# Kernel tuning notes

Hardware: AMD Instinct MI355X
Metric: run time of the kernel (lower is better)

## Reference

```python
import jax, jax.numpy as jnp
import numpy as np

B, N, E, IN = 16, 4096, 65536, 128
FILTERS = [256, 256, 128]


def setup_inputs() -> dict:
    key = jax.random.key(0)
    ks = jax.random.split(key, 12)
    inp = {
        "x": jax.random.normal(ks[0], (B, N, IN), dtype=jnp.float32),
        "edge_index": jax.random.randint(ks[1], (B, 2, E), 0, N, dtype=jnp.int32),
        "edge_weight": jax.random.uniform(ks[2], (B, E), dtype=jnp.float32),
        "mask": jax.random.randint(ks[3], (B, N), 0, 2, dtype=jnp.int32),
    }
    dims = [IN] + FILTERS
    for i in range(3):
        inp[f"W{i+1}"] = jax.random.normal(ks[4 + 2 * i], (dims[i], dims[i + 1]), dtype=jnp.float32) / np.sqrt(dims[i]).astype(np.float32)
        inp[f"b{i+1}"] = 0.01 * jax.random.normal(ks[5 + 2 * i], (dims[i + 1],), dtype=jnp.float32)
    return inp


def _gcn_layer(x, ei, ew, valid, W, b):
    # GCNConv(add_self_loops=False, normalize=False):
    #   h = x @ W; out[v] = sum_{(u,v)} ew * h[u]; out += b (valid rows only)
    h = x @ W  # [N, d_out]
    u, v = ei[0], ei[1]
    evalid = valid[u] & valid[v]            # drop edges touching masked-out nodes
    w = jnp.where(evalid, ew, 0.0)
    agg = jnp.zeros_like(h).at[v].add(w[:, None] * h[u])
    return jnp.where(valid[:, None], agg + b, 0.0)


def reference(x, edge_index, edge_weight, mask, W1, b1, W2, b2, W3, b3):
    valid = mask > 0  # [B, N] bool
    out = x
    for W, b in ((W1, b1), (W2, b2), (W3, b3)):
        out = jax.vmap(_gcn_layer, in_axes=(0, 0, 0, 0, None, None))(
            out, edge_index, edge_weight, valid, W, b)
        out = jax.nn.relu(out)  # dropout p=0.0 -> identity
    return out
```

## Files before the change

kernel.cpp:

```cpp
#include <hip/hip_runtime.h>

static constexpr int BATCH = 16;
static constexpr int NNODE = 4096;
static constexpr int NEDGE = 65536;
static constexpr int ROWS  = BATCH * NNODE;
static constexpr int CAP   = 2432;
static constexpr int PM    = BATCH * CAP;
static constexpr int DCAP  = 64;

typedef _Float16 half8  __attribute__((ext_vector_type(8)));
typedef _Float16 half4v __attribute__((ext_vector_type(4)));
typedef _Float16 half2v __attribute__((ext_vector_type(2)));
typedef float    f32x4  __attribute__((ext_vector_type(4)));
typedef float    f32x2  __attribute__((ext_vector_type(2)));

__global__ __launch_bounds__(256) void build_kernel(
    const int* __restrict__ ei, const float* __restrict__ ew,
    const int* __restrict__ mask, const float* __restrict__ X,
    const float* __restrict__ W1, const float* __restrict__ W2,
    const float* __restrict__ W3,
    int* __restrict__ cursor, unsigned int* __restrict__ bkt,
    _Float16* __restrict__ X16, _Float16* __restrict__ Wt1,
    _Float16* __restrict__ Wt2, _Float16* __restrict__ Wt3,
    int* __restrict__ vlist, int* __restrict__ validN)
{
    __shared__ int sums[256];
    const int blk = blockIdx.x;
    const int t   = threadIdx.x;

    if (blk < 4096) {
        const int idx = blk * 256 + t;
        const int b = idx >> 16;
        const int e = idx & (NEDGE - 1);
        const int* eib = ei + (size_t)b * 2 * NEDGE;
        const int u = eib[e];
        const int v = eib[NEDGE + e];
        const int mrow = b * NNODE;
        if (mask[mrow + u] != 0 && mask[mrow + v] != 0) {
            const _Float16 w = (_Float16)ew[(size_t)b * NEDGE + e];
            const unsigned short wb = __builtin_bit_cast(unsigned short, w);
            const int pos = atomicAdd(&cursor[mrow + v], 1);
            if (pos < DCAP)
                bkt[(size_t)(mrow + v) * DCAP + pos] = ((unsigned)wb << 16) | (unsigned)u;
        }
    } else if (blk < 12288) {
        const int i = (blk - 4096) * 256 + t;
        const int row = i >> 5;
        const int c4  = i & 31;
        const float4 s = *(const float4*)&X[(size_t)row * 128 + c4 * 4];
        half4v h = {(_Float16)s.x, (_Float16)s.y, (_Float16)s.z, (_Float16)s.w};
        *(half4v*)&X16[(size_t)row * 128 + c4 * 4] = h;
    } else if (blk < 12800) {
        const int i = (blk - 12288) * 256 + t;
        if (i < 32768) {
            int k = i >> 8, n = i & 255;
            Wt1[n * 128 + k] = (_Float16)W1[i];
        } else if (i < 98304) {
            int j = i - 32768;
            int k = j >> 8, n = j & 255;
            Wt2[n * 256 + k] = (_Float16)W2[j];
        } else {
            int j = i - 98304;
            int k = j >> 7, n = j & 127;
            Wt3[n * 256 + k] = (_Float16)W3[j];
        }
    } else {
        const int b = blk - 12800;
        const int* mb = mask + b * NNODE;
        for (int i = t; i < CAP; i += 256) vlist[b * CAP + i] = 0;

        int loc[16]; int s = 0;
        #pragma unroll
        for (int i = 0; i < 16; ++i) { loc[i] = (mb[t * 16 + i] != 0); s += loc[i]; }
        sums[t] = s;
        __syncthreads();
        for (int off = 1; off < 256; off <<= 1) {
            int v = (t >= off) ? sums[t - off] : 0;
            __syncthreads();
            sums[t] += v;
            __syncthreads();
        }
        int run = (t == 0) ? 0 : sums[t - 1];
        #pragma unroll
        for (int i = 0; i < 16; ++i) {
            const int n = t * 16 + i;
            if (loc[i]) {
                if (run < CAP) vlist[b * CAP + run] = n;
                ++run;
            }
        }
        if (t == 255) validN[b] = run;
    }
}

__global__ __launch_bounds__(256, 3) void fused_g1(
    const unsigned int* __restrict__ bkt, const int* __restrict__ cursor,
    const _Float16* __restrict__ X16,
    const int* __restrict__ vlist, const int* __restrict__ validN,
    const _Float16* __restrict__ Wt,
    const float* __restrict__ bias,
    _Float16* __restrict__ Ac)
{
    constexpr int K = 128, N = 256;
    constexpr int NPAN = K / 32;
    constexpr int NW   = N / 4;
    constexpr int NI   = NW / 16;
    constexpr int RST  = NW + 8;
    constexpr int NCH  = CAP / 64;
    __shared__ _Float16 A16[NPAN * 2048];

    const int tid  = threadIdx.x;
    const int lane = tid & 63;
    const int wave = tid >> 6;
    const int quad = lane >> 4;
    const int l15  = lane & 15;

    const int xcd  = blockIdx.x & 7;
    const int j    = blockIdx.x >> 3;
    const int batch = 2 * xcd + (j >= NCH);
    const int tile  = (j >= NCH) ? j - NCH : j;
    const int vN   = validN[batch];
    if (tile * 64 >= vN) return;
    const int mrow = batch * NNODE;
    const _Float16* Xb = X16 + (size_t)mrow * 128 + lane * 2;

    for (int r = 0; r < 16; ++r) {
        const int slot = tile * 64 + wave * 16 + r;
        float a0 = 0.0f, a1 = 0.0f;
        if (slot < vN) {
            const int v = vlist[batch * CAP + slot];
            int deg = cursor[mrow + v];
            deg = deg > DCAP ? DCAP : deg;
            const unsigned* bk = bkt + (size_t)(mrow + v) * DCAP;
            for (int i = 0; i < deg; i += 8) {
                const int cnt = deg - i;
                unsigned pk[8];
                #pragma unroll
                for (int tt = 0; tt < 8; ++tt) pk[tt] = bk[i + tt];
                const unsigned u0 = pk[0] & 0xffffu;
                float wj[8]; const _Float16* hp[8];
                #pragma unroll
                for (int tt = 0; tt < 8; ++tt) {
                    const bool ok = (tt < cnt);
                    const unsigned u = ok ? (pk[tt] & 0xffffu) : u0;
                    wj[tt] = ok ? (float)__builtin_bit_cast(_Float16, (unsigned short)(pk[tt] >> 16)) : 0.0f;
                    hp[tt] = Xb + (size_t)u * 128;
                }
                half2v hv[8];
                #pragma unroll
                for (int tt = 0; tt < 8; ++tt) hv[tt] = *(const half2v*)hp[tt];
                #pragma unroll
                for (int tt = 0; tt < 8; ++tt) {
                    a0 += wj[tt] * (float)hv[tt][0];
                    a1 += wj[tt] * (float)hv[tt][1];
                }
            }
        }
        const int row = wave * 16 + r;
        half2v o = {(_Float16)a0, (_Float16)a1};
        *(half2v*)&A16[quad * 2048 + row * 32 + l15 * 2] = o;
    }
    __syncthreads();

    f32x4 acc[4][NI];
    #pragma unroll
    for (int mi = 0; mi < 4; ++mi)
        #pragma unroll
        for (int ni = 0; ni < NI; ++ni) acc[mi][ni] = (f32x4)0.0f;

    const _Float16* ap = A16 + l15 * 32 + quad * 8;
    const _Float16* wp = Wt + (size_t)(wave * NW + l15) * K + quad * 8;

    #pragma unroll
    for (int pp = 0; pp < NPAN; ++pp) {
        half8 af[4], bf[NI];
        #pragma unroll
        for (int mi = 0; mi < 4; ++mi)
            af[mi] = *(const half8*)(ap + pp * 2048 + mi * 16 * 32);
        #pragma unroll
        for (int ni = 0; ni < NI; ++ni)
            bf[ni] = *(const half8*)(wp + (size_t)ni * 16 * K + pp * 32);
        #pragma unroll
        for (int mi = 0; mi < 4; ++mi)
            #pragma unroll
            for (int ni = 0; ni < NI; ++ni)
                acc[mi][ni] = __builtin_amdgcn_mfma_f32_16x16x32_f16(
                    bf[ni], af[mi], acc[mi][ni], 0, 0, 0);
    }
    __syncthreads();

    _Float16* stg = A16 + wave * 16 * RST;
    const int rr = lane >> 2;
    const int c0 = lane & 3;
    #pragma unroll
    for (int mi = 0; mi < 4; ++mi) {
        #pragma unroll
        for (int ni = 0; ni < NI; ++ni) {
            f32x4 v = acc[mi][ni];
            const f32x4 bv = *(const f32x4*)&bias[wave * NW + ni * 16 + quad * 4];
            half4v o;
            #pragma unroll
            for (int r = 0; r < 4; ++r) o[r] = (_Float16)fmaxf(v[r] + bv[r], 0.0f);
            *(half4v*)&stg[l15 * RST + ni * 16 + quad * 4] = o;
        }
        const int slot = tile * 64 + mi * 16 + rr;
        if (slot < vN) {
            const int vs = vlist[batch * CAP + slot];
            _Float16* hp2 = &Ac[((size_t)mrow + vs) * 256 + wave * NW];
            #pragma unroll
            for (int c = 0; c < NI / 2; ++c) {
                const int ch = (c0 + 4 * c) * 8;
                half8 v = *(const half8*)&stg[rr * RST + ch];
                *(half8*)(hp2 + ch) = v;
            }
        }
    }
}

__global__ __launch_bounds__(256, 3) void fused_g23(
    const unsigned int* __restrict__ bkt, const int* __restrict__ cursor,
    const _Float16* __restrict__ Ac,
    const int* __restrict__ vlist, const int* __restrict__ validN,
    const _Float16* __restrict__ Wt2,
    const _Float16* __restrict__ Wt3,
    const float* __restrict__ b2,
    _Float16* __restrict__ H3)
{
    constexpr int K    = 256;
    constexpr int NPAN = 8;
    constexpr int NCH  = CAP / 64;
    __shared__ _Float16 A16[NPAN * 2048];

    const int tid  = threadIdx.x;
    const int lane = tid & 63;
    const int wave = tid >> 6;
    const int quad = lane >> 4;
    const int l15  = lane & 15;

    const int xcd  = blockIdx.x & 7;
    const int j    = blockIdx.x >> 3;
    const int batch = 2 * xcd + (j >= NCH);
    const int tile  = (j >= NCH) ? j - NCH : j;
    const int vN   = validN[batch];
    if (tile * 64 >= vN) return;
    const int mrow = batch * NNODE;
    const _Float16* Ab = Ac + (size_t)mrow * 256 + lane * 4;

    for (int r = 0; r < 16; ++r) {
        const int slot = tile * 64 + wave * 16 + r;
        float a0 = 0.0f, a1 = 0.0f, a2 = 0.0f, a3 = 0.0f;
        if (slot < vN) {
            const int v = vlist[batch * CAP + slot];
            int deg = cursor[mrow + v];
            deg = deg > DCAP ? DCAP : deg;
            const unsigned* bk = bkt + (size_t)(mrow + v) * DCAP;
            for (int i = 0; i < deg; i += 8) {
                const int cnt = deg - i;
                unsigned pk[8];
                #pragma unroll
                for (int tt = 0; tt < 8; ++tt) pk[tt] = bk[i + tt];
                const unsigned u0 = pk[0] & 0xffffu;
                float wj[8]; const _Float16* hp[8];
                #pragma unroll
                for (int tt = 0; tt < 8; ++tt) {
                    const bool ok = (tt < cnt);
                    const unsigned u = ok ? (pk[tt] & 0xffffu) : u0;
                    wj[tt] = ok ? (float)__builtin_bit_cast(_Float16, (unsigned short)(pk[tt] >> 16)) : 0.0f;
                    hp[tt] = Ab + (size_t)u * 256;
                }
                half4v hv[8];
                #pragma unroll
                for (int tt = 0; tt < 8; ++tt) hv[tt] = *(const half4v*)hp[tt];
                #pragma unroll
                for (int tt = 0; tt < 8; ++tt) {
                    a0 += wj[tt] * (float)hv[tt][0];
                    a1 += wj[tt] * (float)hv[tt][1];
                    a2 += wj[tt] * (float)hv[tt][2];
                    a3 += wj[tt] * (float)hv[tt][3];
                }
            }
        }
        const int row = wave * 16 + r;
        half4v o = {(_Float16)a0, (_Float16)a1, (_Float16)a2, (_Float16)a3};
        *(half4v*)&A16[(lane >> 3) * 2048 + row * 32 + ((lane * 4) & 31)] = o;
    }
    __syncthreads();

    f32x4 acc[4][4];
    #pragma unroll
    for (int mi = 0; mi < 4; ++mi)
        #pragma unroll
        for (int ni = 0; ni < 4; ++ni) acc[mi][ni] = (f32x4)0.0f;

    const _Float16* ap = A16 + l15 * 32 + quad * 8;
    const _Float16* wp = Wt2 + (size_t)(wave * 64 + l15) * K + quad * 8;

    #pragma unroll
    for (int pp = 0; pp < NPAN; ++pp) {
        half8 af[4], bf[4];
        #pragma unroll
        for (int mi = 0; mi < 4; ++mi)
            af[mi] = *(const half8*)(ap + pp * 2048 + mi * 16 * 32);
        #pragma unroll
        for (int ni = 0; ni < 4; ++ni)
            bf[ni] = *(const half8*)(wp + (size_t)ni * 16 * K + pp * 32);
        #pragma unroll
        for (int mi = 0; mi < 4; ++mi)
            #pragma unroll
            for (int ni = 0; ni < 4; ++ni)
                acc[mi][ni] = __builtin_amdgcn_mfma_f32_16x16x32_f16(
                    bf[ni], af[mi], acc[mi][ni], 0, 0, 0);
    }
    __syncthreads();

    #pragma unroll
    for (int mi = 0; mi < 4; ++mi) {
        const int row = mi * 16 + l15;
        #pragma unroll
        for (int ni = 0; ni < 4; ++ni) {
            const int col = wave * 64 + ni * 16 + quad * 4;
            const f32x4 bv = *(const f32x4*)&b2[col];
            f32x4 v = acc[mi][ni];
            half4v o;
            #pragma unroll
            for (int r = 0; r < 4; ++r) o[r] = (_Float16)fmaxf(v[r] + bv[r], 0.0f);
            *(half4v*)&A16[(col >> 5) * 2048 + row * 32 + (col & 31)] = o;
        }
    }
    __syncthreads();

    f32x4 acc2[4][2];
    #pragma unroll
    for (int mi = 0; mi < 4; ++mi)
        #pragma unroll
        for (int ni = 0; ni < 2; ++ni) acc2[mi][ni] = (f32x4)0.0f;

    const _Float16* wp3 = Wt3 + (size_t)(wave * 32 + l15) * K + quad * 8;
    #pragma unroll
    for (int pp = 0; pp < NPAN; ++pp) {
        half8 af[4], bf[2];
        #pragma unroll
        for (int mi = 0; mi < 4; ++mi)
            af[mi] = *(const half8*)(ap + pp * 2048 + mi * 16 * 32);
        #pragma unroll
        for (int ni = 0; ni < 2; ++ni)
            bf[ni] = *(const half8*)(wp3 + (size_t)ni * 16 * K + pp * 32);
        #pragma unroll
        for (int mi = 0; mi < 4; ++mi)
            #pragma unroll
            for (int ni = 0; ni < 2; ++ni)
                acc2[mi][ni] = __builtin_amdgcn_mfma_f32_16x16x32_f16(
                    bf[ni], af[mi], acc2[mi][ni], 0, 0, 0);
    }
    __syncthreads();

    constexpr int RST = 40;
    _Float16* stg = A16 + wave * 16 * RST;
    const int rr = lane >> 2;
    const int c0 = lane & 3;
    #pragma unroll
    for (int mi = 0; mi < 4; ++mi) {
        #pragma unroll
        for (int ni = 0; ni < 2; ++ni) {
            f32x4 v = acc2[mi][ni];
            half4v o;
            #pragma unroll
            for (int r = 0; r < 4; ++r) o[r] = (_Float16)v[r];
            *(half4v*)&stg[l15 * RST + ni * 16 + quad * 4] = o;
        }
        const int slot = tile * 64 + mi * 16 + rr;
        if (slot < vN) {
            const int vs = vlist[batch * CAP + slot];
            _Float16* hp2 = &H3[((size_t)mrow + vs) * 128 + wave * 32];
            const int ch = c0 * 8;
            half8 v = *(const half8*)&stg[rr * RST + ch];
            *(half8*)(hp2 + ch) = v;
        }
    }
}

__global__ __launch_bounds__(256) void gather_final(
    const int* __restrict__ cursor, const unsigned int* __restrict__ bkt,
    const _Float16* __restrict__ H3,
    const int* __restrict__ mask, const float* __restrict__ bias,
    float* __restrict__ OUT)
{
    constexpr int NU = NNODE / 4;
    const int tid  = threadIdx.x;
    const int lane = tid & 63;
    const int wave = tid >> 6;

    const int xcd  = blockIdx.x & 7;
    const int jj   = blockIdx.x >> 3;
    const int batch = 2 * xcd + (jj >= NU);
    const int unit  = (jj >= NU) ? jj - NU : jj;

    const int n = unit * 4 + wave;
    const int mrow = batch * NNODE + n;

    float acc[2] = {};
    if (mask[mrow] != 0) {
        int deg = cursor[mrow];
        deg = deg > DCAP ? DCAP : deg;
        const unsigned* bk = bkt + (size_t)mrow * DCAP;
        const _Float16* Hb = H3 + (size_t)batch * NNODE * 128 + lane * 2;

        for (int i = 0; i < deg; i += 8) {
            const int cnt = deg - i;
            unsigned pk[8];
            #pragma unroll
            for (int t = 0; t < 8; ++t) pk[t] = bk[i + t];
            const unsigned u0 = pk[0] & 0xffffu;
            float wj[8]; const _Float16* hp[8];
            #pragma unroll
            for (int t = 0; t < 8; ++t) {
                const bool ok = (t < cnt);
                const unsigned u = ok ? (pk[t] & 0xffffu) : u0;
                wj[t] = ok ? (float)__builtin_bit_cast(_Float16, (unsigned short)(pk[t] >> 16)) : 0.0f;
                hp[t] = Hb + (size_t)u * 128;
            }
            half2v hv[8];
            #pragma unroll
            for (int t = 0; t < 8; ++t) hv[t] = *(const half2v*)hp[t];
            #pragma unroll
            for (int t = 0; t < 8; ++t)
                #pragma unroll
                for (int c = 0; c < 2; ++c) acc[c] += wj[t] * (float)hv[t][c];
        }
        #pragma unroll
        for (int c = 0; c < 2; ++c)
            acc[c] = fmaxf(acc[c] + bias[lane * 2 + c], 0.0f);
    }
    f32x2 o = {acc[0], acc[1]};
    *(f32x2*)&OUT[(size_t)mrow * 128 + lane * 2] = o;
}

extern "C" void kernel_launch(void* const* d_in, const int* in_sizes, int n_in,
                              void* d_out, int out_size, void* d_ws, size_t ws_size,
                              hipStream_t stream) {
    const float* x    = (const float*)d_in[0];
    const int*   ei   = (const int*)  d_in[1];
    const float* ew   = (const float*)d_in[2];
    const int*   mask = (const int*)  d_in[3];
    const float* W1   = (const float*)d_in[4];
    const float* b1   = (const float*)d_in[5];
    const float* W2   = (const float*)d_in[6];
    const float* b2   = (const float*)d_in[7];
    const float* W3   = (const float*)d_in[8];
    const float* b3   = (const float*)d_in[9];
    float* out = (float*)d_out;

    char* ws = (char*)d_ws;
    _Float16* X16 = (_Float16*)(ws);
    _Float16* Ac  = (_Float16*)(ws + (16u << 20));
    _Float16* H3  = (_Float16*)(ws + (48u << 20));
    unsigned int* bkt = (unsigned int*)(ws + (64u << 20));
    _Float16* Wt1 = (_Float16*)(ws + (80u << 20));
    _Float16* Wt2 = Wt1 + 128 * 256;
    _Float16* Wt3 = Wt2 + 256 * 256;
    int* cursor   = (int*)(Wt3 + 256 * 128);
    int* vlist    = cursor + ROWS;
    int* validN   = vlist + PM;

    const dim3 blk(256);

    hipMemsetAsync(cursor, 0, (size_t)ROWS * sizeof(int), stream);

    build_kernel<<<12816, blk, 0, stream>>>(ei, ew, mask, x, W1, W2, W3,
                                            cursor, bkt, X16, Wt1, Wt2, Wt3,
                                            vlist, validN);

    const int gemmBlocks = PM / 64;
    const int finBlocks  = ROWS / 4;

    fused_g1<<<gemmBlocks, blk, 0, stream>>>(bkt, cursor, X16, vlist, validN,
                                             Wt1, b1, Ac);

    fused_g23<<<gemmBlocks, blk, 0, stream>>>(bkt, cursor, Ac, vlist, validN,
                                              Wt2, Wt3, b2, H3);

    gather_final<<<finBlocks, blk, 0, stream>>>(cursor, bkt, H3, mask, b3, out);
}
```

Baseline: 221.5 us.

## Gather fp32 X directly, halve GEMM tile rows, stage bucket heads in LDS

Drops the separate X-to-fp16 conversion pass from the build kernel, so layer 1 gathers fp32 features straight from the input and skips writing and re-reading a 16 MB fp16 copy. Both fused aggregate+GEMM kernels now process 32 rows per block instead of 64, doubling the block count, raising the occupancy hint to 4, and padding LDS panels to reduce bank conflicts. The first 16 bucket entries per row are prefetched into shared memory and gathered in a single unrolled batch, with a scalar tail for higher degrees. The cost is twice as many weight-fragment loads per output row, and wider fp32 gathers in layer 1.

```diff
diff --git a/kernel.cpp b/kernel.cpp
--- a/kernel.cpp
+++ b/kernel.cpp
@@ -16,12 +16,12 @@
 
 __global__ __launch_bounds__(256) void build_kernel(
     const int* __restrict__ ei, const float* __restrict__ ew,
-    const int* __restrict__ mask, const float* __restrict__ X,
+    const int* __restrict__ mask,
     const float* __restrict__ W1, const float* __restrict__ W2,
     const float* __restrict__ W3,
     int* __restrict__ cursor, unsigned int* __restrict__ bkt,
-    _Float16* __restrict__ X16, _Float16* __restrict__ Wt1,
-    _Float16* __restrict__ Wt2, _Float16* __restrict__ Wt3,
+    _Float16* __restrict__ Wt1, _Float16* __restrict__ Wt2,
+    _Float16* __restrict__ Wt3,
     int* __restrict__ vlist, int* __restrict__ validN)
 {
     __shared__ int sums[256];
@@ -43,15 +43,8 @@
             if (pos < DCAP)
                 bkt[(size_t)(mrow + v) * DCAP + pos] = ((unsigned)wb << 16) | (unsigned)u;
         }
-    } else if (blk < 12288) {
+    } else if (blk < 4608) {
         const int i = (blk - 4096) * 256 + t;
-        const int row = i >> 5;
-        const int c4  = i & 31;
-        const float4 s = *(const float4*)&X[(size_t)row * 128 + c4 * 4];
-        half4v h = {(_Float16)s.x, (_Float16)s.y, (_Float16)s.z, (_Float16)s.w};
-        *(half4v*)&X16[(size_t)row * 128 + c4 * 4] = h;
-    } else if (blk < 12800) {
-        const int i = (blk - 12288) * 256 + t;
         if (i < 32768) {
             int k = i >> 8, n = i & 255;
             Wt1[n * 128 + k] = (_Float16)W1[i];
@@ -65,7 +58,7 @@
             Wt3[n * 256 + k] = (_Float16)W3[j];
         }
     } else {
-        const int b = blk - 12800;
+        const int b = blk - 4608;
         const int* mb = mask + b * NNODE;
         for (int i = t; i < CAP; i += 256) vlist[b * CAP + i] = 0;
 
@@ -93,21 +86,23 @@
     }
 }
 
-__global__ __launch_bounds__(256, 3) void fused_g1(
+__global__ __launch_bounds__(256, 4) void fused_g1(
     const unsigned int* __restrict__ bkt, const int* __restrict__ cursor,
-    const _Float16* __restrict__ X16,
+    const float* __restrict__ X,
     const int* __restrict__ vlist, const int* __restrict__ validN,
     const _Float16* __restrict__ Wt,
     const float* __restrict__ bias,
     _Float16* __restrict__ Ac)
 {
-    constexpr int K = 128, N = 256;
-    constexpr int NPAN = K / 32;
-    constexpr int NW   = N / 4;
-    constexpr int NI   = NW / 16;
-    constexpr int RST  = NW + 8;
-    constexpr int NCH  = CAP / 64;
-    __shared__ _Float16 A16[NPAN * 2048];
+    constexpr int K = 128;
+    constexpr int NPAN = 4;
+    constexpr int PSTR = 1032;
+    constexpr int NW = 64, NI = 4, RST = 72;
+    constexpr int NCH = CAP / 32;
+    constexpr int ASZ = (NPAN * PSTR) > (4 * 16 * RST) ? (NPAN * PSTR) : (4 * 16 * RST);
+    __shared__ _Float16 A16[ASZ];
+    __shared__ int s_v[32], s_deg[32];
+    __shared__ unsigned s_bk[32][16];
 
     const int tid  = threadIdx.x;
     const int lane = tid & 63;
@@ -120,51 +115,65 @@
     const int batch = 2 * xcd + (j >= NCH);
     const int tile  = (j >= NCH) ? j - NCH : j;
     const int vN   = validN[batch];
-    if (tile * 64 >= vN) return;
+    if (tile * 32 >= vN) return;
     const int mrow = batch * NNODE;
-    const _Float16* Xb = X16 + (size_t)mrow * 128 + lane * 2;
-
-    for (int r = 0; r < 16; ++r) {
-        const int slot = tile * 64 + wave * 16 + r;
+
+    if (tid < 32) {
+        const int slot = tile * 32 + tid;
+        int v = 0, dg = 0;
+        if (slot < vN) {
+            v = vlist[batch * CAP + slot];
+            dg = cursor[mrow + v];
+            dg = dg > DCAP ? DCAP : dg;
+        }
+        s_v[tid] = v; s_deg[tid] = dg;
+    }
+    __syncthreads();
+    if (tid < 128) {
+        const int r = tid >> 2, part = tid & 3;
+        const uint4 q = *(const uint4*)&bkt[(size_t)(mrow + s_v[r]) * DCAP + part * 4];
+        *(uint4*)&s_bk[r][part * 4] = q;
+    }
+    __syncthreads();
+
+    const float* Xb = X + (size_t)mrow * 128 + lane * 2;
+    for (int r8 = 0; r8 < 8; ++r8) {
+        const int r = wave * 8 + r8;
+        const int dg = s_deg[r];
         float a0 = 0.0f, a1 = 0.0f;
-        if (slot < vN) {
-            const int v = vlist[batch * CAP + slot];
-            int deg = cursor[mrow + v];
-            deg = deg > DCAP ? DCAP : deg;
-            const unsigned* bk = bkt + (size_t)(mrow + v) * DCAP;
-            for (int i = 0; i < deg; i += 8) {
-                const int cnt = deg - i;
-                unsigned pk[8];
-                #pragma unroll
-                for (int tt = 0; tt < 8; ++tt) pk[tt] = bk[i + tt];
-                const unsigned u0 = pk[0] & 0xffffu;
-                float wj[8]; const _Float16* hp[8];
-                #pragma unroll
-                for (int tt = 0; tt < 8; ++tt) {
-                    const bool ok = (tt < cnt);
-                    const unsigned u = ok ? (pk[tt] & 0xffffu) : u0;
-                    wj[tt] = ok ? (float)__builtin_bit_cast(_Float16, (unsigned short)(pk[tt] >> 16)) : 0.0f;
-                    hp[tt] = Xb + (size_t)u * 128;
+        if (dg > 0) {
+            unsigned pk[16];
+            #pragma unroll
+            for (int t = 0; t < 16; ++t) pk[t] = s_bk[r][t];
+            const unsigned u0 = pk[0] & 0xffffu;
+            float wj[16]; float2 xv[16];
+            #pragma unroll
+            for (int t = 0; t < 16; ++t) {
+                const bool ok = (t < dg);
+                const unsigned u = ok ? (pk[t] & 0xffffu) : u0;
+                wj[t] = ok ? (float)__builtin_bit_cast(_Float16, (unsigned short)(pk[t] >> 16)) : 0.0f;
+                xv[t] = *(const float2*)(Xb + (size_t)u * 128);
+            }
+            #pragma unroll
+            for (int t = 0; t < 16; ++t) { a0 += wj[t] * xv[t].x; a1 += wj[t] * xv[t].y; }
+            if (dg > 16) {
+                const unsigned* bk = bkt + (size_t)(mrow + s_v[r]) * DCAP;
+                for (int i = 16; i < dg; ++i) {
+                    const unsigned p = bk[i];
+                    const float w = (float)__builtin_bit_cast(_Float16, (unsigned short)(p >> 16));
+                    const float2 x2 = *(const float2*)(Xb + (size_t)(p & 0xffffu) * 128);
+                    a0 += w * x2.x; a1 += w * x2.y;
                 }
-                half2v hv[8];
-                #pragma unroll
-                for (int tt = 0; tt < 8; ++tt) hv[tt] = *(const half2v*)hp[tt];
-                #pragma unroll
-                for (int tt = 0; tt < 8; ++tt) {
-                    a0 += wj[tt] * (float)hv[tt][0];
-                    a1 += wj[tt] * (float)hv[tt][1];
-                }
-            }
-        }
-        const int row = wave * 16 + r;
+            }
+        }
         half2v o = {(_Float16)a0, (_Float16)a1};
-        *(half2v*)&A16[quad * 2048 + row * 32 + l15 * 2] = o;
-    }
-    __syncthreads();
-
-    f32x4 acc[4][NI];
-    #pragma unroll
-    for (int mi = 0; mi < 4; ++mi)
+        *(half2v*)&A16[(lane >> 4) * PSTR + r * 32 + ((lane * 2) & 31)] = o;
+    }
+    __syncthreads();
+
+    f32x4 acc[2][NI];
+    #pragma unroll
+    for (int mi = 0; mi < 2; ++mi)
         #pragma unroll
         for (int ni = 0; ni < NI; ++ni) acc[mi][ni] = (f32x4)0.0f;
 
@@ -173,15 +182,15 @@
 
     #pragma unroll
     for (int pp = 0; pp < NPAN; ++pp) {
-        half8 af[4], bf[NI];
-        #pragma unroll
-        for (int mi = 0; mi < 4; ++mi)
-            af[mi] = *(const half8*)(ap + pp * 2048 + mi * 16 * 32);
+        half8 af[2], bf[NI];
+        #pragma unroll
+        for (int mi = 0; mi < 2; ++mi)
+            af[mi] = *(const half8*)(ap + pp * PSTR + mi * 16 * 32);
         #pragma unroll
         for (int ni = 0; ni < NI; ++ni)
             bf[ni] = *(const half8*)(wp + (size_t)ni * 16 * K + pp * 32);
         #pragma unroll
-        for (int mi = 0; mi < 4; ++mi)
+        for (int mi = 0; mi < 2; ++mi)
             #pragma unroll
             for (int ni = 0; ni < NI; ++ni)
                 acc[mi][ni] = __builtin_amdgcn_mfma_f32_16x16x32_f16(
@@ -193,7 +202,7 @@
     const int rr = lane >> 2;
     const int c0 = lane & 3;
     #pragma unroll
-    for (int mi = 0; mi < 4; ++mi) {
+    for (int mi = 0; mi < 2; ++mi) {
         #pragma unroll
         for (int ni = 0; ni < NI; ++ni) {
             f32x4 v = acc[mi][ni];
@@ -203,9 +212,9 @@
             for (int r = 0; r < 4; ++r) o[r] = (_Float16)fmaxf(v[r] + bv[r], 0.0f);
             *(half4v*)&stg[l15 * RST + ni * 16 + quad * 4] = o;
         }
-        const int slot = tile * 64 + mi * 16 + rr;
+        const int slot = tile * 32 + mi * 16 + rr;
         if (slot < vN) {
-            const int vs = vlist[batch * CAP + slot];
+            const int vs = s_v[mi * 16 + rr];
             _Float16* hp2 = &Ac[((size_t)mrow + vs) * 256 + wave * NW];
             #pragma unroll
             for (int c = 0; c < NI / 2; ++c) {
@@ -217,7 +226,7 @@
     }
 }
 
-__global__ __launch_bounds__(256, 3) void fused_g23(
+__global__ __launch_bounds__(256, 4) void fused_g23(
     const unsigned int* __restrict__ bkt, const int* __restrict__ cursor,
     const _Float16* __restrict__ Ac,
     const int* __restrict__ vlist, const int* __restrict__ validN,
@@ -228,8 +237,11 @@
 {
     constexpr int K    = 256;
     constexpr int NPAN = 8;
-    constexpr int NCH  = CAP / 64;
-    __shared__ _Float16 A16[NPAN * 2048];
+    constexpr int PSTR = 1032;
+    constexpr int NCH  = CAP / 32;
+    __shared__ _Float16 A16[NPAN * PSTR];
+    __shared__ int s_v[32], s_deg[32];
+    __shared__ unsigned s_bk[32][16];
 
     const int tid  = threadIdx.x;
     const int lane = tid & 63;
@@ -242,53 +254,71 @@
     const int batch = 2 * xcd + (j >= NCH);
     const int tile  = (j >= NCH) ? j - NCH : j;
     const int vN   = validN[batch];
-    if (tile * 64 >= vN) return;
+    if (tile * 32 >= vN) return;
     const int mrow = batch * NNODE;
+
+    if (tid < 32) {
+        const int slot = tile * 32 + tid;
+        int v = 0, dg = 0;
+        if (slot < vN) {
+            v = vlist[batch * CAP + slot];
+            dg = cursor[mrow + v];
+            dg = dg > DCAP ? DCAP : dg;
+        }
+        s_v[tid] = v; s_deg[tid] = dg;
+    }
+    __syncthreads();
+    if (tid < 128) {
+        const int r = tid >> 2, part = tid & 3;
+        const uint4 q = *(const uint4*)&bkt[(size_t)(mrow + s_v[r]) * DCAP + part * 4];
+        *(uint4*)&s_bk[r][part * 4] = q;
+    }
+    __syncthreads();
+
     const _Float16* Ab = Ac + (size_t)mrow * 256 + lane * 4;
-
-    for (int r = 0; r < 16; ++r) {
-        const int slot = tile * 64 + wave * 16 + r;
+    for (int r8 = 0; r8 < 8; ++r8) {
+        const int r = wave * 8 + r8;
+        const int dg = s_deg[r];
         float a0 = 0.0f, a1 = 0.0f, a2 = 0.0f, a3 = 0.0f;
-        if (slot < vN) {
-            const int v = vlist[batch * CAP + slot];
-            int deg = cursor[mrow + v];
-            deg = deg > DCAP ? DCAP : deg;
-            const unsigned* bk = bkt + (size_t)(mrow + v) * DCAP;
-            for (int i = 0; i < deg; i += 8) {
-                const int cnt = deg - i;
-                unsigned pk[8];
-                #pragma unroll
-                for (int tt = 0; tt < 8; ++tt) pk[tt] = bk[i + tt];
-                const unsigned u0 = pk[0] & 0xffffu;
-                float wj[8]; const _Float16* hp[8];
-                #pragma unroll
-                for (int tt = 0; tt < 8; ++tt) {
-                    const bool ok = (tt < cnt);
-                    const unsigned u = ok ? (pk[tt] & 0xffffu) : u0;
-                    wj[tt] = ok ? (float)__builtin_bit_cast(_Float16, (unsigned short)(pk[tt] >> 16)) : 0.0f;
-                    hp[tt] = Ab + (size_t)u * 256;
+        if (dg > 0) {
+            unsigned pk[16];
+            #pragma unroll
+            for (int t = 0; t < 16; ++t) pk[t] = s_bk[r][t];
+            const unsigned u0 = pk[0] & 0xffffu;
+            float wj[16]; half4v hv[16];
+            #pragma unroll
+            for (int t = 0; t < 16; ++t) {
+                const bool ok = (t < dg);
+                const unsigned u = ok ? (pk[t] & 0xffffu) : u0;
+                wj[t] = ok ? (float)__builtin_bit_cast(_Float16, (unsigned short)(pk[t] >> 16)) : 0.0f;
+                hv[t] = *(const half4v*)(Ab + (size_t)u * 256);
+            }
+            #pragma unroll
+            for (int t = 0; t < 16; ++t) {
+                a0 += wj[t] * (float)hv[t][0];
+                a1 += wj[t] * (float)hv[t][1];
+                a2 += wj[t] * (float)hv[t][2];
+                a3 += wj[t] * (float)hv[t][3];
+            }
+            if (dg > 16) {
+                const unsigned* bk = bkt + (size_t)(mrow + s_v[r]) * DCAP;
+                for (int i = 16; i < dg; ++i) {
+                    const unsigned p = bk[i];
+                    const float w = (float)__builtin_bit_cast(_Float16, (unsigned short)(p >> 16));
+                    const half4v h = *(const half4v*)(Ab + (size_t)(p & 0xffffu) * 256);
+                    a0 += w * (float)h[0]; a1 += w * (float)h[1];
+                    a2 += w * (float)h[2]; a3 += w * (float)h[3];
                 }
-                half4v hv[8];
-                #pragma unroll
-                for (int tt = 0; tt < 8; ++tt) hv[tt] = *(const half4v*)hp[tt];
-                #pragma unroll
-                for (int tt = 0; tt < 8; ++tt) {
-                    a0 += wj[tt] * (float)hv[tt][0];
-                    a1 += wj[tt] * (float)hv[tt][1];
-                    a2 += wj[tt] * (float)hv[tt][2];
-                    a3 += wj[tt] * (float)hv[tt][3];
-                }
-            }
-        }
-        const int row = wave * 16 + r;
+            }
+        }
         half4v o = {(_Float16)a0, (_Float16)a1, (_Float16)a2, (_Float16)a3};
-        *(half4v*)&A16[(lane >> 3) * 2048 + row * 32 + ((lane * 4) & 31)] = o;
-    }
-    __syncthreads();
-
-    f32x4 acc[4][4];
-    #pragma unroll
-    for (int mi = 0; mi < 4; ++mi)
+        *(half4v*)&A16[(lane >> 3) * PSTR + r * 32 + ((lane * 4) & 31)] = o;
+    }
+    __syncthreads();
+
+    f32x4 acc[2][4];
+    #pragma unroll
+    for (int mi = 0; mi < 2; ++mi)
         #pragma unroll
         for (int ni = 0; ni < 4; ++ni) acc[mi][ni] = (f32x4)0.0f;
 
@@ -297,15 +327,15 @@
 
     #pragma unroll
     for (int pp = 0; pp < NPAN; ++pp) {
-        half8 af[4], bf[4];
-        #pragma unroll
-        for (int mi = 0; mi < 4; ++mi)
-            af[mi] = *(const half8*)(ap + pp * 2048 + mi * 16 * 32);
+        half8 af[2], bf[4];
+        #pragma unroll
+        for (int mi = 0; mi < 2; ++mi)
+            af[mi] = *(const half8*)(ap + pp * PSTR + mi * 16 * 32);
         #pragma unroll
         for (int ni = 0; ni < 4; ++ni)
             bf[ni] = *(const half8*)(wp + (size_t)ni * 16 * K + pp * 32);
         #pragma unroll
-        for (int mi = 0; mi < 4; ++mi)
+        for (int mi = 0; mi < 2; ++mi)
             #pragma unroll
             for (int ni = 0; ni < 4; ++ni)
                 acc[mi][ni] = __builtin_amdgcn_mfma_f32_16x16x32_f16(
@@ -314,7 +344,7 @@
     __syncthreads();
 
     #pragma unroll
-    for (int mi = 0; mi < 4; ++mi) {
+    for (int mi = 0; mi < 2; ++mi) {
         const int row = mi * 16 + l15;
         #pragma unroll
         for (int ni = 0; ni < 4; ++ni) {
@@ -324,29 +354,29 @@
             half4v o;
             #pragma unroll
             for (int r = 0; r < 4; ++r) o[r] = (_Float16)fmaxf(v[r] + bv[r], 0.0f);
-            *(half4v*)&A16[(col >> 5) * 2048 + row * 32 + (col & 31)] = o;
-        }
-    }
-    __syncthreads();
-
-    f32x4 acc2[4][2];
-    #pragma unroll
-    for (int mi = 0; mi < 4; ++mi)
+            *(half4v*)&A16[(col >> 5) * PSTR + row * 32 + (col & 31)] = o;
+        }
+    }
+    __syncthreads();
+
+    f32x4 acc2[2][2];
+    #pragma unroll
+    for (int mi = 0; mi < 2; ++mi)
         #pragma unroll
         for (int ni = 0; ni < 2; ++ni) acc2[mi][ni] = (f32x4)0.0f;
 
     const _Float16* wp3 = Wt3 + (size_t)(wave * 32 + l15) * K + quad * 8;
     #pragma unroll
     for (int pp = 0; pp < NPAN; ++pp) {
-        half8 af[4], bf[2];
-        #pragma unroll
-        for (int mi = 0; mi < 4; ++mi)
-            af[mi] = *(const half8*)(ap + pp * 2048 + mi * 16 * 32);
+        half8 af[2], bf[2];
+        #pragma unroll
+        for (int mi = 0; mi < 2; ++mi)
+            af[mi] = *(const half8*)(ap + pp * PSTR + mi * 16 * 32);
         #pragma unroll
         for (int ni = 0; ni < 2; ++ni)
             bf[ni] = *(const half8*)(wp3 + (size_t)ni * 16 * K + pp * 32);
         #pragma unroll
-        for (int mi = 0; mi < 4; ++mi)
+        for (int mi = 0; mi < 2; ++mi)
             #pragma unroll
             for (int ni = 0; ni < 2; ++ni)
                 acc2[mi][ni] = __builtin_amdgcn_mfma_f32_16x16x32_f16(
@@ -359,7 +389,7 @@
     const int rr = lane >> 2;
     const int c0 = lane & 3;
     #pragma unroll
-    for (int mi = 0; mi < 4; ++mi) {
+    for (int mi = 0; mi < 2; ++mi) {
         #pragma unroll
         for (int ni = 0; ni < 2; ++ni) {
             f32x4 v = acc2[mi][ni];
@@ -368,9 +398,9 @@
             for (int r = 0; r < 4; ++r) o[r] = (_Float16)v[r];
             *(half4v*)&stg[l15 * RST + ni * 16 + quad * 4] = o;
         }
-        const int slot = tile * 64 + mi * 16 + rr;
+        const int slot = tile * 32 + mi * 16 + rr;
         if (slot < vN) {
-            const int vs = vlist[batch * CAP + slot];
+            const int vs = s_v[mi * 16 + rr];
             _Float16* hp2 = &H3[((size_t)mrow + vs) * 128 + wave * 32];
             const int ch = c0 * 8;
             half8 v = *(const half8*)&stg[rr * RST + ch];
@@ -451,11 +481,10 @@
     float* out = (float*)d_out;
 
     char* ws = (char*)d_ws;
-    _Float16* X16 = (_Float16*)(ws);
-    _Float16* Ac  = (_Float16*)(ws + (16u << 20));
-    _Float16* H3  = (_Float16*)(ws + (48u << 20));
-    unsigned int* bkt = (unsigned int*)(ws + (64u << 20));
-    _Float16* Wt1 = (_Float16*)(ws + (80u << 20));
+    _Float16* Ac  = (_Float16*)(ws);
+    _Float16* H3  = (_Float16*)(ws + (32u << 20));
+    unsigned int* bkt = (unsigned int*)(ws + (48u << 20));
+    _Float16* Wt1 = (_Float16*)(ws + (64u << 20));
     _Float16* Wt2 = Wt1 + 128 * 256;
     _Float16* Wt3 = Wt2 + 256 * 256;
     int* cursor   = (int*)(Wt3 + 256 * 128);
@@ -466,14 +495,14 @@
 
     hipMemsetAsync(cursor, 0, (size_t)ROWS * sizeof(int), stream);
 
-    build_kernel<<<12816, blk, 0, stream>>>(ei, ew, mask, x, W1, W2, W3,
-                                            cursor, bkt, X16, Wt1, Wt2, Wt3,
-                                            vlist, validN);
-
-    const int gemmBlocks = PM / 64;
+    build_kernel<<<4624, blk, 0, stream>>>(ei, ew, mask, W1, W2, W3,
+                                           cursor, bkt, Wt1, Wt2, Wt3,
+                                           vlist, validN);
+
+    const int gemmBlocks = PM / 32;
     const int finBlocks  = ROWS / 4;
 
-    fused_g1<<<gemmBlocks, blk, 0, stream>>>(bkt, cursor, X16, vlist, validN,
+    fused_g1<<<gemmBlocks, blk, 0, stream>>>(bkt, cursor, x, vlist, validN,
                                              Wt1, b1, Ac);
 
     fused_g23<<<gemmBlocks, blk, 0, stream>>>(bkt, cursor, Ac, vlist, validN,
```

After: 220.7 us. Within noise of the previous version (-0.3%).

## Split neighbor gather out of fused GEMM kernels into separate gather passes

Applied to the files above, without the earlier changes.

Each fused gather+GEMM kernel is split in two. A standalone gather kernel (one wave per valid node) writes the aggregated rows to a compact buffer. The GEMM kernel then loads that buffer into LDS with global_load_lds, and vlist lookups are cached in shared memory. The fp32-to-fp16 conversion of X is removed: the first gather reads fp32 X directly, and the build kernel shrinks to match. Padding lanes now load index-masked rows instead of duplicating the first neighbor. This spreads the latency-bound gather across many more waves, in exchange for two extra launches and an HBM round trip for the aggregated intermediates.

```diff
diff --git a/kernel.cpp b/kernel.cpp
--- a/kernel.cpp
+++ b/kernel.cpp
@@ -14,14 +14,17 @@
 typedef float    f32x4  __attribute__((ext_vector_type(4)));
 typedef float    f32x2  __attribute__((ext_vector_type(2)));
 
+#define GP(p) (const __attribute__((address_space(1))) void*)(p)
+#define LP(p) (__attribute__((address_space(3))) void*)(p)
+
 __global__ __launch_bounds__(256) void build_kernel(
     const int* __restrict__ ei, const float* __restrict__ ew,
-    const int* __restrict__ mask, const float* __restrict__ X,
+    const int* __restrict__ mask,
     const float* __restrict__ W1, const float* __restrict__ W2,
     const float* __restrict__ W3,
     int* __restrict__ cursor, unsigned int* __restrict__ bkt,
-    _Float16* __restrict__ X16, _Float16* __restrict__ Wt1,
-    _Float16* __restrict__ Wt2, _Float16* __restrict__ Wt3,
+    _Float16* __restrict__ Wt1, _Float16* __restrict__ Wt2,
+    _Float16* __restrict__ Wt3,
     int* __restrict__ vlist, int* __restrict__ validN)
 {
     __shared__ int sums[256];
@@ -43,15 +46,8 @@
             if (pos < DCAP)
                 bkt[(size_t)(mrow + v) * DCAP + pos] = ((unsigned)wb << 16) | (unsigned)u;
         }
-    } else if (blk < 12288) {
+    } else if (blk < 4608) {
         const int i = (blk - 4096) * 256 + t;
-        const int row = i >> 5;
-        const int c4  = i & 31;
-        const float4 s = *(const float4*)&X[(size_t)row * 128 + c4 * 4];
-        half4v h = {(_Float16)s.x, (_Float16)s.y, (_Float16)s.z, (_Float16)s.w};
-        *(half4v*)&X16[(size_t)row * 128 + c4 * 4] = h;
-    } else if (blk < 12800) {
-        const int i = (blk - 12288) * 256 + t;
         if (i < 32768) {
             int k = i >> 8, n = i & 255;
             Wt1[n * 128 + k] = (_Float16)W1[i];
@@ -65,7 +61,7 @@
             Wt3[n * 256 + k] = (_Float16)W3[j];
         }
     } else {
-        const int b = blk - 12800;
+        const int b = blk - 4608;
         const int* mb = mask + b * NNODE;
         for (int i = t; i < CAP; i += 256) vlist[b * CAP + i] = 0;
 
@@ -93,21 +89,113 @@
     }
 }
 
-__global__ __launch_bounds__(256, 3) void fused_g1(
-    const unsigned int* __restrict__ bkt, const int* __restrict__ cursor,
-    const _Float16* __restrict__ X16,
+
+__global__ __launch_bounds__(256) void gather_x(
+    const int* __restrict__ cursor, const unsigned int* __restrict__ bkt,
+    const float* __restrict__ X,
+    const int* __restrict__ vlist, const int* __restrict__ validN,
+    _Float16* __restrict__ AggX)
+{
+    constexpr int NU = CAP / 4;
+    const int lane = threadIdx.x & 63;
+    const int wave = threadIdx.x >> 6;
+    const int xcd  = blockIdx.x & 7;
+    const int jj   = blockIdx.x >> 3;
+    const int batch = 2 * xcd + (jj >= NU);
+    const int unit  = (jj >= NU) ? jj - NU : jj;
+
+    const int j = unit * 4 + wave;
+    if (j >= validN[batch]) return;
+    const int mrow = batch * NNODE;
+    const int v = vlist[batch * CAP + j];
+    int deg = cursor[mrow + v];
+    deg = deg > DCAP ? DCAP : deg;
+    const unsigned* bk = bkt + (size_t)(mrow + v) * DCAP;
+    const float* Xb = X + (size_t)mrow * 128 + lane * 2;
+
+    float a0 = 0.0f, a1 = 0.0f;
+    for (int i = 0; i < deg; i += 8) {
+        const int cnt = deg - i;
+        unsigned pk[8];
+        #pragma unroll
+        for (int t = 0; t < 8; ++t) pk[t] = bk[i + t];
+        float wj[8]; float2 xv[8];
+        #pragma unroll
+        for (int t = 0; t < 8; ++t) {
+            const bool ok = (t < cnt);
+            const unsigned u = pk[t] & 0xFFFu;
+            wj[t] = ok ? (float)__builtin_bit_cast(_Float16, (unsigned short)(pk[t] >> 16)) : 0.0f;
+            xv[t] = *(const float2*)(Xb + (size_t)u * 128);
+        }
+        #pragma unroll
+        for (int t = 0; t < 8; ++t) { a0 += wj[t] * xv[t].x; a1 += wj[t] * xv[t].y; }
+    }
+    half2v o = {(_Float16)a0, (_Float16)a1};
+    *(half2v*)&AggX[(size_t)(batch * CAP + j) * 128 + lane * 2] = o;
+}
+
+__global__ __launch_bounds__(256) void gather_agg(
+    const int* __restrict__ cursor, const unsigned int* __restrict__ bkt,
+    const _Float16* __restrict__ Ac,
+    const int* __restrict__ vlist, const int* __restrict__ validN,
+    _Float16* __restrict__ AggA)
+{
+    constexpr int NU = CAP / 4;
+    const int lane = threadIdx.x & 63;
+    const int wave = threadIdx.x >> 6;
+    const int xcd  = blockIdx.x & 7;
+    const int jj   = blockIdx.x >> 3;
+    const int batch = 2 * xcd + (jj >= NU);
+    const int unit  = (jj >= NU) ? jj - NU : jj;
+
+    const int j = unit * 4 + wave;
+    if (j >= validN[batch]) return;
+    const int mrow = batch * NNODE;
+    const int v = vlist[batch * CAP + j];
+    int deg = cursor[mrow + v];
+    deg = deg > DCAP ? DCAP : deg;
+    const unsigned* bk = bkt + (size_t)(mrow + v) * DCAP;
+    const _Float16* Ab = Ac + (size_t)mrow * 256 + lane * 4;
+
+    float a0 = 0.0f, a1 = 0.0f, a2 = 0.0f, a3 = 0.0f;
+    for (int i = 0; i < deg; i += 8) {
+        const int cnt = deg - i;
+        unsigned pk[8];
+        #pragma unroll
+        for (int t = 0; t < 8; ++t) pk[t] = bk[i + t];
+        float wj[8]; half4v hv[8];
+        #pragma unroll
+        for (int t = 0; t < 8; ++t) {
+            const bool ok = (t < cnt);
+            const unsigned u = pk[t] & 0xFFFu;
+            wj[t] = ok ? (float)__builtin_bit_cast(_Float16, (unsigned short)(pk[t] >> 16)) : 0.0f;
+            hv[t] = *(const half4v*)(Ab + (size_t)u * 256);
+        }
+        #pragma unroll
+        for (int t = 0; t < 8; ++t) {
+            a0 += wj[t] * (float)hv[t][0];
+            a1 += wj[t] * (float)hv[t][1];
+            a2 += wj[t] * (float)hv[t][2];
+            a3 += wj[t] * (float)hv[t][3];
+        }
+    }
+    half4v o = {(_Float16)a0, (_Float16)a1, (_Float16)a2, (_Float16)a3};
+    *(half4v*)&AggA[(size_t)(batch * CAP + j) * 256 + lane * 4] = o;
+}
+
+__global__ __launch_bounds__(256, 3) void gemm1_kernel(
+    const _Float16* __restrict__ Xc,
     const int* __restrict__ vlist, const int* __restrict__ validN,
     const _Float16* __restrict__ Wt,
     const float* __restrict__ bias,
     _Float16* __restrict__ Ac)
 {
-    constexpr int K = 128, N = 256;
-    constexpr int NPAN = K / 32;
-    constexpr int NW   = N / 4;
-    constexpr int NI   = NW / 16;
-    constexpr int RST  = NW + 8;
+    constexpr int K = 128, NW = 64, NI = 4, RST = 72;
+    constexpr int NPAN = 4;
     constexpr int NCH  = CAP / 64;
-    __shared__ _Float16 A16[NPAN * 2048];
+    constexpr int ASZ  = (NPAN * 2048) > (4 * 16 * RST) ? (NPAN * 2048) : (4 * 16 * RST);
+    __shared__ _Float16 A16[ASZ];
+    __shared__ int s_v[64];
 
     const int tid  = threadIdx.x;
     const int lane = tid & 63;
@@ -122,44 +210,19 @@
     const int vN   = validN[batch];
     if (tile * 64 >= vN) return;
     const int mrow = batch * NNODE;
-    const _Float16* Xb = X16 + (size_t)mrow * 128 + lane * 2;
-
-    for (int r = 0; r < 16; ++r) {
-        const int slot = tile * 64 + wave * 16 + r;
-        float a0 = 0.0f, a1 = 0.0f;
-        if (slot < vN) {
-            const int v = vlist[batch * CAP + slot];
-            int deg = cursor[mrow + v];
-            deg = deg > DCAP ? DCAP : deg;
-            const unsigned* bk = bkt + (size_t)(mrow + v) * DCAP;
-            for (int i = 0; i < deg; i += 8) {
-                const int cnt = deg - i;
-                unsigned pk[8];
-                #pragma unroll
-                for (int tt = 0; tt < 8; ++tt) pk[tt] = bk[i + tt];
-                const unsigned u0 = pk[0] & 0xffffu;
-                float wj[8]; const _Float16* hp[8];
-                #pragma unroll
-                for (int tt = 0; tt < 8; ++tt) {
-                    const bool ok = (tt < cnt);
-                    const unsigned u = ok ? (pk[tt] & 0xffffu) : u0;
-                    wj[tt] = ok ? (float)__builtin_bit_cast(_Float16, (unsigned short)(pk[tt] >> 16)) : 0.0f;
-                    hp[tt] = Xb + (size_t)u * 128;
-                }
-                half2v hv[8];
-                #pragma unroll
-                for (int tt = 0; tt < 8; ++tt) hv[tt] = *(const half2v*)hp[tt];
-                #pragma unroll
-                for (int tt = 0; tt < 8; ++tt) {
-                    a0 += wj[tt] * (float)hv[tt][0];
-                    a1 += wj[tt] * (float)hv[tt][1];
-                }
-            }
-        }
-        const int row = wave * 16 + r;
-        half2v o = {(_Float16)a0, (_Float16)a1};
-        *(half2v*)&A16[quad * 2048 + row * 32 + l15 * 2] = o;
-    }
+    const size_t bm = (size_t)batch * CAP + (size_t)tile * 64;
+
+    if (tid < 64) {
+        const int slot = tile * 64 + tid;
+        s_v[tid] = (slot < vN) ? vlist[batch * CAP + slot] : 0;
+    }
+    const int srow = tid >> 2;
+    const int sch  = (tid & 3) * 8;
+    #pragma unroll
+    for (int pp = 0; pp < NPAN; ++pp)
+        __builtin_amdgcn_global_load_lds(
+            GP(Xc + (bm + srow) * K + pp * 32 + sch),
+            LP(A16 + pp * 2048 + tid * 8), 16, 0, 0);
     __syncthreads();
 
     f32x4 acc[4][NI];
@@ -205,7 +268,7 @@
         }
         const int slot = tile * 64 + mi * 16 + rr;
         if (slot < vN) {
-            const int vs = vlist[batch * CAP + slot];
+            const int vs = s_v[mi * 16 + rr];
             _Float16* hp2 = &Ac[((size_t)mrow + vs) * 256 + wave * NW];
             #pragma unroll
             for (int c = 0; c < NI / 2; ++c) {
@@ -217,9 +280,8 @@
     }
 }
 
-__global__ __launch_bounds__(256, 3) void fused_g23(
-    const unsigned int* __restrict__ bkt, const int* __restrict__ cursor,
-    const _Float16* __restrict__ Ac,
+__global__ __launch_bounds__(256, 3) void gemm23_kernel(
+    const _Float16* __restrict__ Xc,
     const int* __restrict__ vlist, const int* __restrict__ validN,
     const _Float16* __restrict__ Wt2,
     const _Float16* __restrict__ Wt3,
@@ -230,6 +292,7 @@
     constexpr int NPAN = 8;
     constexpr int NCH  = CAP / 64;
     __shared__ _Float16 A16[NPAN * 2048];
+    __shared__ int s_v[64];
 
     const int tid  = threadIdx.x;
     const int lane = tid & 63;
@@ -244,46 +307,19 @@
     const int vN   = validN[batch];
     if (tile * 64 >= vN) return;
     const int mrow = batch * NNODE;
-    const _Float16* Ab = Ac + (size_t)mrow * 256 + lane * 4;
-
-    for (int r = 0; r < 16; ++r) {
-        const int slot = tile * 64 + wave * 16 + r;
-        float a0 = 0.0f, a1 = 0.0f, a2 = 0.0f, a3 = 0.0f;
-        if (slot < vN) {
-            const int v = vlist[batch * CAP + slot];
-            int deg = cursor[mrow + v];
-            deg = deg > DCAP ? DCAP : deg;
-            const unsigned* bk = bkt + (size_t)(mrow + v) * DCAP;
-            for (int i = 0; i < deg; i += 8) {
-                const int cnt = deg - i;
-                unsigned pk[8];
-                #pragma unroll
-                for (int tt = 0; tt < 8; ++tt) pk[tt] = bk[i + tt];
-                const unsigned u0 = pk[0] & 0xffffu;
-                float wj[8]; const _Float16* hp[8];
-                #pragma unroll
-                for (int tt = 0; tt < 8; ++tt) {
-                    const bool ok = (tt < cnt);
-                    const unsigned u = ok ? (pk[tt] & 0xffffu) : u0;
-                    wj[tt] = ok ? (float)__builtin_bit_cast(_Float16, (unsigned short)(pk[tt] >> 16)) : 0.0f;
-                    hp[tt] = Ab + (size_t)u * 256;
-                }
-                half4v hv[8];
-                #pragma unroll
-                for (int tt = 0; tt < 8; ++tt) hv[tt] = *(const half4v*)hp[tt];
-                #pragma unroll
-                for (int tt = 0; tt < 8; ++tt) {
-                    a0 += wj[tt] * (float)hv[tt][0];
-                    a1 += wj[tt] * (float)hv[tt][1];
-                    a2 += wj[tt] * (float)hv[tt][2];
-                    a3 += wj[tt] * (float)hv[tt][3];
-                }
-            }
-        }
-        const int row = wave * 16 + r;
-        half4v o = {(_Float16)a0, (_Float16)a1, (_Float16)a2, (_Float16)a3};
-        *(half4v*)&A16[(lane >> 3) * 2048 + row * 32 + ((lane * 4) & 31)] = o;
-    }
+    const size_t bm = (size_t)batch * CAP + (size_t)tile * 64;
+
+    if (tid < 64) {
+        const int slot = tile * 64 + tid;
+        s_v[tid] = (slot < vN) ? vlist[batch * CAP + slot] : 0;
+    }
+    const int srow = tid >> 2;
+    const int sch  = (tid & 3) * 8;
+    #pragma unroll
+    for (int pp = 0; pp < NPAN; ++pp)
+        __builtin_amdgcn_global_load_lds(
+            GP(Xc + (bm + srow) * K + pp * 32 + sch),
+            LP(A16 + pp * 2048 + tid * 8), 16, 0, 0);
     __syncthreads();
 
     f32x4 acc[4][4];
@@ -370,7 +406,7 @@
         }
         const int slot = tile * 64 + mi * 16 + rr;
         if (slot < vN) {
-            const int vs = vlist[batch * CAP + slot];
+            const int vs = s_v[mi * 16 + rr];
             _Float16* hp2 = &H3[((size_t)mrow + vs) * 128 + wave * 32];
             const int ch = c0 * 8;
             half8 v = *(const half8*)&stg[rr * RST + ch];
@@ -386,9 +422,8 @@
     float* __restrict__ OUT)
 {
     constexpr int NU = NNODE / 4;
-    const int tid  = threadIdx.x;
-    const int lane = tid & 63;
-    const int wave = tid >> 6;
+    const int lane = threadIdx.x & 63;
+    const int wave = threadIdx.x >> 6;
 
     const int xcd  = blockIdx.x & 7;
     const int jj   = blockIdx.x >> 3;
@@ -410,12 +445,11 @@
             unsigned pk[8];
             #pragma unroll
             for (int t = 0; t < 8; ++t) pk[t] = bk[i + t];
-            const unsigned u0 = pk[0] & 0xffffu;
             float wj[8]; const _Float16* hp[8];
             #pragma unroll
             for (int t = 0; t < 8; ++t) {
                 const bool ok = (t < cnt);
-                const unsigned u = ok ? (pk[t] & 0xffffu) : u0;
+                const unsigned u = pk[t] & 0xFFFu;
                 wj[t] = ok ? (float)__builtin_bit_cast(_Float16, (unsigned short)(pk[t] >> 16)) : 0.0f;
                 hp[t] = Hb + (size_t)u * 128;
             }
@@ -451,33 +485,35 @@
     float* out = (float*)d_out;
 
     char* ws = (char*)d_ws;
-    _Float16* X16 = (_Float16*)(ws);
-    _Float16* Ac  = (_Float16*)(ws + (16u << 20));
-    _Float16* H3  = (_Float16*)(ws + (48u << 20));
-    unsigned int* bkt = (unsigned int*)(ws + (64u << 20));
-    _Float16* Wt1 = (_Float16*)(ws + (80u << 20));
-    _Float16* Wt2 = Wt1 + 128 * 256;
-    _Float16* Wt3 = Wt2 + 256 * 256;
-    int* cursor   = (int*)(Wt3 + 256 * 128);
-    int* vlist    = cursor + ROWS;
-    int* validN   = vlist + PM;
+    _Float16* Ac   = (_Float16*)(ws);
+    _Float16* H3   = (_Float16*)(ws + (32u << 20));
+    unsigned int* bkt = (unsigned int*)(ws + (48u << 20));
+    _Float16* AggX = (_Float16*)(ws + (64u << 20));
+    _Float16* AggA = (_Float16*)(ws + (74u << 20));
+    _Float16* Wt1  = (_Float16*)(ws + (94u << 20));
+    _Float16* Wt2  = Wt1 + 128 * 256;
+    _Float16* Wt3  = Wt2 + 256 * 256;
+    int* cursor    = (int*)(Wt3 + 256 * 128);
+    int* vlist     = cursor + ROWS;
+    int* validN    = vlist + PM;
 
     const dim3 blk(256);
 
     hipMemsetAsync(cursor, 0, (size_t)ROWS * sizeof(int), stream);
 
-    build_kernel<<<12816, blk, 0, stream>>>(ei, ew, mask, x, W1, W2, W3,
-                                            cursor, bkt, X16, Wt1, Wt2, Wt3,
-                                            vlist, validN);
+    build_kernel<<<4624, blk, 0, stream>>>(ei, ew, mask, W1, W2, W3,
+                                           cursor, bkt, Wt1, Wt2, Wt3,
+                                           vlist, validN);
 
     const int gemmBlocks = PM / 64;
+    const int aggBlocks  = PM / 4;
     const int finBlocks  = ROWS / 4;
 
-    fused_g1<<<gemmBlocks, blk, 0, stream>>>(bkt, cursor, X16, vlist, validN,
-                                             Wt1, b1, Ac);
-
-    fused_g23<<<gemmBlocks, blk, 0, stream>>>(bkt, cursor, Ac, vlist, validN,
-                                              Wt2, Wt3, b2, H3);
+    gather_x<<<aggBlocks, blk, 0, stream>>>(cursor, bkt, x, vlist, validN, AggX);
+    gemm1_kernel<<<gemmBlocks, blk, 0, stream>>>(AggX, vlist, validN, Wt1, b1, Ac);
+
+    gather_agg<<<aggBlocks, blk, 0, stream>>>(cursor, bkt, Ac, vlist, validN, AggA);
+    gemm23_kernel<<<gemmBlocks, blk, 0, stream>>>(AggA, vlist, validN, Wt2, Wt3, b2, H3);
 
     gather_final<<<finBlocks, blk, 0, stream>>>(cursor, bkt, H3, mask, b3, out);
 }
```

Result: faster. 208.4 us (-5.9%).
